# Performance work log

Measured on AMD Instinct MI355X. Metric: run time of the kernel, lower is better.

## Reference

```python
import jax, jax.numpy as jnp
import numpy as np

B, T, C, H = 2, 2048, 768, 12
HD = C // H  # head dim = 64
EPS = 1e-5


def layer_norm(x, g, b):
    mu = jnp.mean(x, axis=-1, keepdims=True)
    var = jnp.var(x, axis=-1, keepdims=True)
    return (x - mu) * jax.lax.rsqrt(var + EPS) * g + b


def setup_inputs() -> dict:
    key = jax.random.key(0)
    ks = jax.random.split(key, 5)
    s = 0.02
    return {
        "x": jax.random.normal(ks[0], (B, T, C), jnp.float32),
        "ln1_g": jnp.ones((C,), jnp.float32),
        "ln1_b": jnp.zeros((C,), jnp.float32),
        "W_qkv": jax.random.normal(ks[1], (C, 3 * C), jnp.float32) * s,
        "W_attn_proj": jax.random.normal(ks[2], (C, C), jnp.float32) * s,
        "ln2_g": jnp.ones((C,), jnp.float32),
        "ln2_b": jnp.zeros((C,), jnp.float32),
        "W_fc": jax.random.normal(ks[3], (C, 4 * C), jnp.float32) * s,
        "W_mlp_proj": jax.random.normal(ks[4], (4 * C, C), jnp.float32) * s,
    }


def attention(x, W_qkv, W_attn_proj):
    b, t, c = x.shape
    qkv = x @ W_qkv  # [B,T,3C]
    q, k, v = jnp.split(qkv, 3, axis=-1)
    # [B,H,T,HD]
    q = q.reshape(b, t, H, HD).transpose(0, 2, 1, 3)
    k = k.reshape(b, t, H, HD).transpose(0, 2, 1, 3)
    v = v.reshape(b, t, H, HD).transpose(0, 2, 1, 3)
    att = jnp.einsum("bhqd,bhkd->bhqk", q, k) * (1.0 / np.sqrt(HD).astype(np.float32))
    causal = jnp.tril(jnp.ones((t, t), jnp.bool_))
    att = jnp.where(causal, att, jnp.finfo(att.dtype).min)
    att = jax.nn.softmax(att, axis=-1)
    y = jnp.einsum("bhqk,bhkd->bhqd", att, v)
    y = y.transpose(0, 2, 1, 3).reshape(b, t, c)
    return y @ W_attn_proj


def mlp(x, W_fc, W_mlp_proj):
    h = jax.nn.gelu(x @ W_fc, approximate=False)
    return h @ W_mlp_proj


def reference(x, ln1_g, ln1_b, W_qkv, W_attn_proj, ln2_g, ln2_b, W_fc, W_mlp_proj):
    x = x + attention(layer_norm(x, ln1_g, ln1_b), W_qkv, W_attn_proj)
    x = x + mlp(layer_norm(x, ln2_g, ln2_b), W_fc, W_mlp_proj)
    return x
```

## Files before the change

kernel.cpp:

```cpp
#include <hip/hip_runtime.h>
#include <cstdint>
#include <cstddef>

typedef unsigned short u16;
typedef __attribute__((ext_vector_type(4))) float f32x4;
typedef __attribute__((ext_vector_type(8))) short bf16x8;

__device__ __forceinline__ u16 f2bf(float f) {
  unsigned int u = __builtin_bit_cast(unsigned int, f);
  u += 0x7fffu + ((u >> 16) & 1u);
  return (u16)(u >> 16);
}

__device__ __forceinline__ void gl_lds16(const u16* g, u16* lds_base) {
  __builtin_amdgcn_global_load_lds(
      (const __attribute__((address_space(1))) unsigned int*)g,
      (__attribute__((address_space(3))) unsigned int*)lds_base, 16, 0, 0);
}

__global__ __launch_bounds__(256) void transpose_all(const float* __restrict__ s0,
                                                     const float* __restrict__ s1,
                                                     const float* __restrict__ s2,
                                                     const float* __restrict__ s3,
                                                     u16* __restrict__ d0,
                                                     u16* __restrict__ d1,
                                                     u16* __restrict__ d2,
                                                     u16* __restrict__ d3) {
  __shared__ float tile[32][33];
  int idx = blockIdx.x;
  const float* src; u16* dst; int K, N, t;
  if (idx < 1728)      { src = s0; dst = d0; K = 768;  N = 2304; t = idx; }
  else if (idx < 2304) { src = s1; dst = d1; K = 768;  N = 768;  t = idx - 1728; }
  else if (idx < 4608) { src = s2; dst = d2; K = 768;  N = 3072; t = idx - 2304; }
  else                 { src = s3; dst = d3; K = 3072; N = 768;  t = idx - 4608; }
  int nt_n = N >> 5;
  int n0 = (t % nt_n) * 32, k0 = (t / nt_n) * 32;
  int tx = threadIdx.x & 31, ty = threadIdx.x >> 5;
#pragma unroll
  for (int i = 0; i < 4; ++i)
    tile[ty + i * 8][tx] = src[(size_t)(k0 + ty + i * 8) * N + n0 + tx];
  __syncthreads();
#pragma unroll
  for (int i = 0; i < 4; ++i)
    dst[(size_t)(n0 + ty + i * 8) * K + k0 + tx] = f2bf(tile[tx][ty + i * 8]);
}

__global__ __launch_bounds__(256) void transpose_v(const u16* __restrict__ qkvb,
                                                   u16* __restrict__ vt,
                                                   unsigned int* __restrict__ ctr) {
  __shared__ u16 tile[64 * 72];
  if (blockIdx.x == 0 && blockIdx.y == 0 && threadIdx.x == 0) *ctr = 0u;
  int t0 = blockIdx.x * 64;
  int bh = blockIdx.y;
  int b = bh / 12, h = bh % 12;
  int tid = threadIdx.x;
  int c8 = tid & 7, r = tid >> 3;
#pragma unroll
  for (int i = 0; i < 2; ++i) {
    int rr = r + i * 32;
    *(uint4*)&tile[rr * 72 + c8 * 8] =
        *(const uint4*)&qkvb[(size_t)(b * 2048 + t0 + rr) * 2304 + 1536 + h * 64 + c8 * 8];
  }
  __syncthreads();
#pragma unroll
  for (int i = 0; i < 2; ++i) {
    int dr = r + i * 32;
    u16 tmp[8];
#pragma unroll
    for (int j = 0; j < 8; ++j) tmp[j] = tile[(c8 * 8 + j) * 72 + dr];
    *(uint4*)&vt[((size_t)bh * 64 + dr) * 2048 + t0 + c8 * 8] = *(uint4*)tmp;
  }
}

__global__ __launch_bounds__(192) void ln_rows(const float* __restrict__ x,
                                               const float* __restrict__ g,
                                               const float* __restrict__ bb,
                                               u16* __restrict__ out) {
  int row = blockIdx.x;
  int t = threadIdx.x;
  float4 v = *(const float4*)(x + (size_t)row * 768 + t * 4);
  float s = v.x + v.y + v.z + v.w;
  float sq = v.x * v.x + v.y * v.y + v.z * v.z + v.w * v.w;
#pragma unroll
  for (int o = 32; o > 0; o >>= 1) {
    s += __shfl_down(s, o);
    sq += __shfl_down(sq, o);
  }
  __shared__ float ss[3], s2[3];
  int w = t >> 6;
  if ((t & 63) == 0) { ss[w] = s; s2[w] = sq; }
  __syncthreads();
  s = ss[0] + ss[1] + ss[2];
  sq = s2[0] + s2[1] + s2[2];
  float mu = s * (1.f / 768.f);
  float var = sq * (1.f / 768.f) - mu * mu;
  float rs = rsqrtf(var + 1e-5f);
  float4 gv = *(const float4*)(g + t * 4);
  float4 bv = *(const float4*)(bb + t * 4);
  u16 o4[4];
  o4[0] = f2bf((v.x - mu) * rs * gv.x + bv.x);
  o4[1] = f2bf((v.y - mu) * rs * gv.y + bv.y);
  o4[2] = f2bf((v.z - mu) * rs * gv.z + bv.z);
  o4[3] = f2bf((v.w - mu) * rs * gv.w + bv.w);
  *(uint2*)(out + (size_t)row * 768 + t * 4) = *(uint2*)o4;
}

template <int EPI, int TM>
__global__ __launch_bounds__(256, 3) void gemm_bt(const u16* __restrict__ A,
                                                  const u16* __restrict__ BT,
                                                  int M, int N, int K,
                                                  float* __restrict__ outF,
                                                  u16* __restrict__ outB,
                                                  const float* __restrict__ res) {
  constexpr int MT = TM / 64;
  __shared__ __align__(16) u16 Al[2][TM * 64];
  __shared__ __align__(16) u16 Bl[2][64 * 64];
  int tid = threadIdx.x;
  int lane = tid & 63, w = tid >> 6;
  int l16 = lane & 15, quad = lane >> 4;
  int swz = l16 & 7;

  int gx = gridDim.x;
  int nwg = gx * gridDim.y;
  int wg = blockIdx.y * gx + blockIdx.x;
  int chunk = nwg >> 3;
  int swg = (wg & 7) * chunk + (wg >> 3);
  int bx = swg % gx, by = swg / gx;

  size_t rowA0 = (size_t)by * TM;
  size_t rowB0 = (size_t)bx * 64;

  auto stage = [&](int buf, int k0) {
#pragma unroll
    for (int i = 0; i < TM / 32; ++i) {
      int cbase = (i * 4 + w) * 64;
      int chunk2 = cbase + lane;
      int r = chunk2 >> 3, c8 = (chunk2 & 7) ^ (r & 7);
      gl_lds16(&A[(rowA0 + r) * (size_t)K + k0 + c8 * 8], &Al[buf][cbase * 8]);
    }
#pragma unroll
    for (int i = 0; i < 2; ++i) {
      int cbase = (i * 4 + w) * 64;
      int chunk2 = cbase + lane;
      int r = chunk2 >> 3, c8 = (chunk2 & 7) ^ (r & 7);
      gl_lds16(&BT[(rowB0 + r) * (size_t)K + k0 + c8 * 8], &Bl[buf][cbase * 8]);
    }
  };

  f32x4 acc[MT][4] = {};
  stage(0, 0);
  int cur = 0;
  for (int k0 = 0; k0 < K; k0 += 64) {
    __syncthreads();
    if (k0 + 64 < K) stage(cur ^ 1, k0 + 64);
#pragma unroll
    for (int ks = 0; ks < 2; ++ks) {
      int c = ks * 4 + quad;
      bf16x8 af[MT], bf[4];
#pragma unroll
      for (int mt = 0; mt < MT; ++mt)
        af[mt] = *(const bf16x8*)&Al[cur][(w * (TM / 4) + mt * 16 + l16) * 64 + (c ^ swz) * 8];
#pragma unroll
      for (int nt = 0; nt < 4; ++nt)
        bf[nt] = *(const bf16x8*)&Bl[cur][(nt * 16 + l16) * 64 + (c ^ swz) * 8];
#pragma unroll
      for (int mt = 0; mt < MT; ++mt)
#pragma unroll
        for (int nt = 0; nt < 4; ++nt)
          acc[mt][nt] = __builtin_amdgcn_mfma_f32_16x16x32_bf16(af[mt], bf[nt], acc[mt][nt], 0, 0, 0);
    }
    cur ^= 1;
  }

#pragma unroll
  for (int mt = 0; mt < MT; ++mt) {
#pragma unroll
    for (int i = 0; i < 4; ++i) {
      size_t row = rowA0 + w * (TM / 4) + mt * 16 + quad * 4 + i;
#pragma unroll
      for (int nt = 0; nt < 4; ++nt) {
        size_t col = rowB0 + nt * 16 + l16;
        float v = acc[mt][nt][i];
        if (EPI == 0) {
          outB[row * N + col] = f2bf(v);
        } else if (EPI == 1) {
          outF[row * N + col] = res[row * N + col] + v;
        } else {
          float ge = 0.5f * v * (1.f + erff(v * 0.70710678118654752f));
          outB[row * N + col] = f2bf(ge);
        }
      }
    }
  }
}

__global__ __launch_bounds__(256, 3) void flash_attn(const u16* __restrict__ qkv,
                                                     const u16* __restrict__ vt,
                                                     u16* __restrict__ y,
                                                     float* __restrict__ OP,
                                                     float* __restrict__ LP,
                                                     unsigned int* __restrict__ ctr) {
  __shared__ __align__(16) u16 Kl[128 * 64];
  __shared__ __align__(16) u16 Vl[64 * 128];
  __shared__ __align__(16) u16 Pl[4][16 * 136];
  __shared__ unsigned int s_unit;

  int tid = threadIdx.x;
  int lane = tid & 63, w = tid >> 6;
  int l16 = lane & 15, quad = lane >> 4;
  int swz = l16 & 7;
  u16* Pw = &Pl[w][0];

  for (;;) {
    __syncthreads();
    if (tid == 0) s_unit = atomicAdd(ctr, 1u);
    __syncthreads();
    unsigned int u = s_unit;
    if (u >= 1152u) return;

    int qt, bh, kb0, kb1, part;
    bool heavy;
    if (u < 384u) {
      int t = (int)u;
      qt = 31 - t / 24; bh = t % 24;
      part = 0; kb0 = 0; kb1 = 8; heavy = true;
    } else if (u < 768u) {
      int t = (int)u - 384;
      qt = 31 - t / 24; bh = t % 24;
      part = 1; kb0 = 8; kb1 = qt / 2 + 1; heavy = true;
    } else {
      int t = (int)u - 768;
      qt = 15 - t / 24; bh = t % 24;
      part = 0; kb0 = 0; kb1 = qt / 2 + 1; heavy = false;
    }
    int b = bh / 12, h = bh % 12;
    int qw = qt * 64 + w * 16;
    int kdiag = qt / 2;

    const u16* base = qkv + (size_t)b * 2048 * 2304;
    const u16* vbase = vt + (size_t)bh * 64 * 2048;

    bf16x8 qf0, qf1;
    {
      const u16* qp = base + (size_t)(qw + l16) * 2304 + h * 64 + quad * 8;
      qf0 = *(const bf16x8*)qp;
      qf1 = *(const bf16x8*)(qp + 32);
    }

    f32x4 O[4] = {};
    float l_i[4] = {0.f, 0.f, 0.f, 0.f};

    const float sc = 0.125f * 1.44269504088896340736f;

    auto stageK = [&](int kt0) {
#pragma unroll
      for (int i = 0; i < 4; ++i) {
        int cbase = (i * 4 + w) * 64;
        int chunk = cbase + lane;
        int r = chunk >> 3, c8 = (chunk & 7) ^ (r & 7);
        gl_lds16(base + (size_t)(kt0 + r) * 2304 + 768 + h * 64 + c8 * 8, &Kl[cbase * 8]);
      }
    };
    auto stageV = [&](int kt0) {
#pragma unroll
      for (int i = 0; i < 4; ++i) {
        int cbase = (i * 4 + w) * 64;
        int chunk = cbase + lane;
        int r = chunk >> 4, c16 = (chunk & 15) ^ (r & 7);
        gl_lds16(vbase + (size_t)r * 2048 + kt0 + c16 * 8, &Vl[cbase * 8]);
      }
    };

    stageK(kb0 << 7);
    for (int kb = kb0; kb < kb1; ++kb) {
      int kt0 = kb << 7;
      __syncthreads();
      stageV(kt0);

      f32x4 S[8];
#pragma unroll
      for (int nt = 0; nt < 8; ++nt) {
        bf16x8 k0 = *(const bf16x8*)&Kl[(nt * 16 + l16) * 64 + (quad ^ swz) * 8];
        bf16x8 k1 = *(const bf16x8*)&Kl[(nt * 16 + l16) * 64 + ((4 + quad) ^ swz) * 8];
        f32x4 z = {};
        z = __builtin_amdgcn_mfma_f32_16x16x32_bf16(qf0, k0, z, 0, 0, 0);
        S[nt] = __builtin_amdgcn_mfma_f32_16x16x32_bf16(qf1, k1, z, 0, 0, 0);
      }

      bool diag = (kb == kdiag);
#pragma unroll
      for (int nt = 0; nt < 8; ++nt) {
        int tk = kt0 + nt * 16 + l16;
#pragma unroll
        for (int i = 0; i < 4; ++i) {
          float p = exp2f(S[nt][i] * sc);
          if (diag && tk > qw + quad * 4 + i) p = 0.f;
          l_i[i] += p;
          Pw[(quad * 4 + i) * 136 + nt * 16 + l16] =
              (u16)(__builtin_bit_cast(unsigned int, p) >> 16);
        }
      }

      __syncthreads();
      if (kb + 1 < kb1) stageK((kb + 1) << 7);

#pragma unroll
      for (int c = 0; c < 4; ++c) {
        bf16x8 pf = *(const bf16x8*)&Pw[l16 * 136 + c * 32 + quad * 8];
#pragma unroll
        for (int dt = 0; dt < 4; ++dt) {
          bf16x8 vf = *(const bf16x8*)&Vl[(dt * 16 + l16) * 128 + ((c * 4 + quad) ^ swz) * 8];
          O[dt] = __builtin_amdgcn_mfma_f32_16x16x32_bf16(pf, vf, O[dt], 0, 0, 0);
        }
      }
    }

#pragma unroll
    for (int i = 0; i < 4; ++i) {
#pragma unroll
      for (int o = 1; o < 16; o <<= 1) l_i[i] += __shfl_xor(l_i[i], o);
    }

    if (heavy) {
      size_t tno = (size_t)(bh * 16 + (qt - 16)) * 2 + part;
      float* op = OP + tno * 4096;
      float* lp = LP + tno * 64;
#pragma unroll
      for (int dt = 0; dt < 4; ++dt) {
#pragma unroll
        for (int i = 0; i < 4; ++i)
          op[(w * 16 + quad * 4 + i) * 64 + dt * 16 + l16] = O[dt][i];
      }
      if (l16 == 0) {
#pragma unroll
        for (int i = 0; i < 4; ++i) lp[w * 16 + quad * 4 + i] = l_i[i];
      }
    } else {
#pragma unroll
      for (int dt = 0; dt < 4; ++dt) {
#pragma unroll
        for (int i = 0; i < 4; ++i) {
          int tq = qw + quad * 4 + i;
          float ov = O[dt][i] / l_i[i];
          y[(size_t)(b * 2048 + tq) * 768 + h * 64 + dt * 16 + l16] = f2bf(ov);
        }
      }
    }
  }
}

__global__ __launch_bounds__(256) void attn_combine(const float* __restrict__ OP,
                                                    const float* __restrict__ LP,
                                                    u16* __restrict__ y) {
  int t = blockIdx.x;
  int bh = t >> 4, qth = t & 15;
  int b = bh / 12, h = bh % 12;
  int tid = threadIdx.x;
  int r = tid >> 2;
  int c0 = (tid & 3) << 4;
  const float* a = OP + (size_t)t * 2 * 4096 + r * 64 + c0;
  const float* bp = a + 4096;
  float inv = 1.f / (LP[(size_t)t * 128 + r] + LP[(size_t)t * 128 + 64 + r]);
  u16 ob[16];
#pragma unroll
  for (int j = 0; j < 16; ++j) ob[j] = f2bf((a[j] + bp[j]) * inv);
  size_t row = (size_t)b * 2048 + (size_t)(16 + qth) * 64 + r;
  u16* yp = y + row * 768 + h * 64 + c0;
  *(uint4*)yp = *(uint4*)&ob[0];
  *(uint4*)(yp + 8) = *(uint4*)&ob[8];
}

extern "C" void kernel_launch(void* const* d_in, const int* in_sizes, int n_in,
                              void* d_out, int out_size, void* d_ws, size_t ws_size,
                              hipStream_t stream) {
  const float* x      = (const float*)d_in[0];
  const float* ln1_g  = (const float*)d_in[1];
  const float* ln1_b  = (const float*)d_in[2];
  const float* W_qkv  = (const float*)d_in[3];
  const float* W_attn = (const float*)d_in[4];
  const float* ln2_g  = (const float*)d_in[5];
  const float* ln2_b  = (const float*)d_in[6];
  const float* W_fc   = (const float*)d_in[7];
  const float* W_mlp  = (const float*)d_in[8];
  float* out = (float*)d_out;

  const int M = 4096;
  char* p = (char*)d_ws;
  auto alloc = [&](size_t bytes) {
    char* r = p;
    p += (bytes + 255) & ~(size_t)255;
    return r;
  };
  u16* wt_qkv  = (u16*)alloc((size_t)2304 * 768 * 2);
  u16* wt_attn = (u16*)alloc((size_t)768 * 768 * 2);
  u16* wt_fc   = (u16*)alloc((size_t)3072 * 768 * 2);
  u16* wt_mlp  = (u16*)alloc((size_t)768 * 3072 * 2);
  u16* xn1     = (u16*)alloc((size_t)M * 768 * 2);
  u16* qkvb    = (u16*)alloc((size_t)M * 2304 * 2);
  u16* yb      = (u16*)alloc((size_t)M * 768 * 2);
  float* x1    = (float*)alloc((size_t)M * 768 * 4);
  u16* xn2     = (u16*)alloc((size_t)M * 768 * 2);
  u16* hb      = (u16*)alloc((size_t)M * 3072 * 2);
  u16* vt      = (u16*)alloc((size_t)24 * 64 * 2048 * 2);
  unsigned int* ctr = (unsigned int*)alloc(256);

  float* OPb = (float*)hb;
  float* LPb = OPb + (size_t)24 * 16 * 2 * 4096;

  transpose_all<<<6912, 256, 0, stream>>>(W_qkv, W_attn, W_fc, W_mlp,
                                          wt_qkv, wt_attn, wt_fc, wt_mlp);

  ln_rows<<<M, 192, 0, stream>>>(x, ln1_g, ln1_b, xn1);
  gemm_bt<0, 128><<<dim3(2304 / 64, M / 128), 256, 0, stream>>>(xn1, wt_qkv, M, 2304, 768,
                                                                nullptr, qkvb, nullptr);
  transpose_v<<<dim3(32, 24), 256, 0, stream>>>(qkvb, vt, ctr);
  flash_attn<<<768, 256, 0, stream>>>(qkvb, vt, yb, OPb, LPb, ctr);
  attn_combine<<<384, 256, 0, stream>>>(OPb, LPb, yb);
  gemm_bt<1, 64><<<dim3(768 / 64, M / 64), 256, 0, stream>>>(yb, wt_attn, M, 768, 768,
                                                             x1, nullptr, x);
  ln_rows<<<M, 192, 0, stream>>>(x1, ln2_g, ln2_b, xn2);
  gemm_bt<2, 128><<<dim3(3072 / 64, M / 128), 256, 0, stream>>>(xn2, wt_fc, M, 3072, 768,
                                                                nullptr, hb, nullptr);
  gemm_bt<1, 64><<<dim3(768 / 64, M / 64), 256, 0, stream>>>(hb, wt_mlp, M, 768, 3072,
                                                             out, nullptr, x1);
}
```

Baseline: 267.6 us.

## Add 128x128 tiled GEMM with XCD-aware block swizzle for QKV and FC projections

Introduces a new gemm_sq kernel that uses 128x128 output tiles with a 2x2 wave layout, so each wave computes a 64x64 sub-tile. It also remaps workgroup IDs into eight chunks so neighbouring tiles land on the same XCD, which should improve L2 reuse. The QKV and FC projections switch to this kernel, halving the grid size and increasing data reuse per loaded tile. The trade-off is more accumulator registers per thread and fewer workgroups, which may reduce occupancy and tail balance on 256 CUs.

```diff
diff --git a/kernel.cpp b/kernel.cpp
--- a/kernel.cpp
+++ b/kernel.cpp
@@ -185,6 +185,91 @@
           outB[row * N + col] = f2bf(v);
         } else if (EPI == 1) {
           outF[row * N + col] = res[row * N + col] + v;
+        } else {
+          float ge = 0.5f * v * (1.f + erff(v * 0.70710678118654752f));
+          outB[row * N + col] = f2bf(ge);
+        }
+      }
+    }
+  }
+}
+
+template <int EPI>
+__global__ __launch_bounds__(256, 2) void gemm_sq(const u16* __restrict__ A,
+                                                  const u16* __restrict__ BT,
+                                                  int M, int N, int K,
+                                                  u16* __restrict__ outB) {
+  __shared__ __align__(16) u16 Al[2][128 * 64];
+  __shared__ __align__(16) u16 Bl[2][128 * 64];
+  int tid = threadIdx.x;
+  int lane = tid & 63, w = tid >> 6;
+  int l16 = lane & 15, quad = lane >> 4;
+  int swz = l16 & 7;
+  int wr = w >> 1, wc = w & 1;
+
+  int gx = gridDim.x;
+  int nwg = gx * gridDim.y;
+  int wg = blockIdx.y * gx + blockIdx.x;
+  int chunk = nwg >> 3;
+  int swg = (wg & 7) * chunk + (wg >> 3);
+  int bx = swg % gx, by = swg / gx;
+
+  size_t rowA0 = (size_t)by * 128;
+  size_t rowB0 = (size_t)bx * 128;
+
+  auto stage = [&](int buf, int k0) {
+#pragma unroll
+    for (int i = 0; i < 4; ++i) {
+      int cbase = (i * 4 + w) * 64;
+      int chunk2 = cbase + lane;
+      int r = chunk2 >> 3, c8 = (chunk2 & 7) ^ (r & 7);
+      gl_lds16(&A[(rowA0 + r) * (size_t)K + k0 + c8 * 8], &Al[buf][cbase * 8]);
+    }
+#pragma unroll
+    for (int i = 0; i < 4; ++i) {
+      int cbase = (i * 4 + w) * 64;
+      int chunk2 = cbase + lane;
+      int r = chunk2 >> 3, c8 = (chunk2 & 7) ^ (r & 7);
+      gl_lds16(&BT[(rowB0 + r) * (size_t)K + k0 + c8 * 8], &Bl[buf][cbase * 8]);
+    }
+  };
+
+  f32x4 acc[4][4] = {};
+  stage(0, 0);
+  int cur = 0;
+  for (int k0 = 0; k0 < K; k0 += 64) {
+    __syncthreads();
+    if (k0 + 64 < K) stage(cur ^ 1, k0 + 64);
+#pragma unroll
+    for (int ks = 0; ks < 2; ++ks) {
+      int c = ks * 4 + quad;
+      bf16x8 af[4], bf[4];
+#pragma unroll
+      for (int mt = 0; mt < 4; ++mt)
+        af[mt] = *(const bf16x8*)&Al[cur][(wr * 64 + mt * 16 + l16) * 64 + (c ^ swz) * 8];
+#pragma unroll
+      for (int nt = 0; nt < 4; ++nt)
+        bf[nt] = *(const bf16x8*)&Bl[cur][(wc * 64 + nt * 16 + l16) * 64 + (c ^ swz) * 8];
+#pragma unroll
+      for (int mt = 0; mt < 4; ++mt)
+#pragma unroll
+        for (int nt = 0; nt < 4; ++nt)
+          acc[mt][nt] = __builtin_amdgcn_mfma_f32_16x16x32_bf16(af[mt], bf[nt], acc[mt][nt], 0, 0, 0);
+    }
+    cur ^= 1;
+  }
+
+#pragma unroll
+  for (int mt = 0; mt < 4; ++mt) {
+#pragma unroll
+    for (int i = 0; i < 4; ++i) {
+      size_t row = rowA0 + wr * 64 + mt * 16 + quad * 4 + i;
+#pragma unroll
+      for (int nt = 0; nt < 4; ++nt) {
+        size_t col = rowB0 + wc * 64 + nt * 16 + l16;
+        float v = acc[mt][nt][i];
+        if (EPI == 0) {
+          outB[row * N + col] = f2bf(v);
         } else {
           float ge = 0.5f * v * (1.f + erff(v * 0.70710678118654752f));
           outB[row * N + col] = f2bf(ge);
@@ -411,16 +496,16 @@
                                           wt_qkv, wt_attn, wt_fc, wt_mlp);
 
   ln_rows<<<M, 192, 0, stream>>>(x, ln1_g, ln1_b, xn1);
-  gemm_bt<0, 128><<<dim3(2304 / 64, M / 128), 256, 0, stream>>>(xn1, wt_qkv, M, 2304, 768,
-                                                                nullptr, qkvb, nullptr);
+  gemm_sq<0><<<dim3(2304 / 128, M / 128), 256, 0, stream>>>(xn1, wt_qkv, M, 2304, 768,
+                                                            qkvb);
   transpose_v<<<dim3(32, 24), 256, 0, stream>>>(qkvb, vt, ctr);
   flash_attn<<<768, 256, 0, stream>>>(qkvb, vt, yb, OPb, LPb, ctr);
   attn_combine<<<384, 256, 0, stream>>>(OPb, LPb, yb);
   gemm_bt<1, 64><<<dim3(768 / 64, M / 64), 256, 0, stream>>>(yb, wt_attn, M, 768, 768,
                                                              x1, nullptr, x);
   ln_rows<<<M, 192, 0, stream>>>(x1, ln2_g, ln2_b, xn2);
-  gemm_bt<2, 128><<<dim3(3072 / 64, M / 128), 256, 0, stream>>>(xn2, wt_fc, M, 3072, 768,
-                                                                nullptr, hb, nullptr);
+  gemm_sq<2><<<dim3(3072 / 128, M / 128), 256, 0, stream>>>(xn2, wt_fc, M, 3072, 768,
+                                                            hb);
   gemm_bt<1, 64><<<dim3(768 / 64, M / 64), 256, 0, stream>>>(hb, wt_mlp, M, 768, 3072,
                                                              out, nullptr, x1);
 }
```

New measurement: 276.3 us. 1.03x slower.

## Shrink flash-attention key tiles to 64 and split-K into 512-key chunks

Applied to the files above, without the earlier changes.

Flash attention now processes 64-key blocks instead of 128, so causal diagonal work is masked at a finer grain and less of it is wasted. Long query tiles (qt≥8) are split into up to four 512-key partial units, with a new schedule ordering work units and a combine kernel that sums up to four partials. The smaller LDS footprint allows raising the occupancy hint from 3 to 6 blocks, and the grid is doubled. In exchange there are more partial writes and reads of fp32 outputs, more scheduling atomics, and more loop iterations with per-iteration barriers. The partial buffer is moved to span the x1/xn2/hb workspace.

```diff
diff --git a/kernel.cpp b/kernel.cpp
--- a/kernel.cpp
+++ b/kernel.cpp
@@ -194,15 +194,15 @@
   }
 }
 
-__global__ __launch_bounds__(256, 3) void flash_attn(const u16* __restrict__ qkv,
+__global__ __launch_bounds__(256, 6) void flash_attn(const u16* __restrict__ qkv,
                                                      const u16* __restrict__ vt,
                                                      u16* __restrict__ y,
                                                      float* __restrict__ OP,
                                                      float* __restrict__ LP,
                                                      unsigned int* __restrict__ ctr) {
-  __shared__ __align__(16) u16 Kl[128 * 64];
-  __shared__ __align__(16) u16 Vl[64 * 128];
-  __shared__ __align__(16) u16 Pl[4][16 * 136];
+  __shared__ __align__(16) u16 Kl[64 * 64];
+  __shared__ __align__(16) u16 Vl[64 * 64];
+  __shared__ __align__(16) u16 Pl[4][16 * 72];
   __shared__ unsigned int s_unit;
 
   int tid = threadIdx.x;
@@ -216,26 +216,27 @@
     if (tid == 0) s_unit = atomicAdd(ctr, 1u);
     __syncthreads();
     unsigned int u = s_unit;
-    if (u >= 1152u) return;
-
-    int qt, bh, kb0, kb1, part;
-    bool heavy;
-    if (u < 384u) {
-      int t = (int)u;
-      qt = 31 - t / 24; bh = t % 24;
-      part = 0; kb0 = 0; kb1 = 8; heavy = true;
-    } else if (u < 768u) {
-      int t = (int)u - 384;
-      qt = 31 - t / 24; bh = t % 24;
-      part = 1; kb0 = 8; kb1 = qt / 2 + 1; heavy = true;
+    if (u >= 1920u) return;
+
+    int qt, bh, kb0, kb1, j;
+    if (u < 1248u) {
+      bh = (int)(u % 24u);
+      int fi = (int)(u / 24u);
+      qt = 31;
+      for (;;) { int nf = (qt + 1) >> 3; if (fi < nf) break; fi -= nf; --qt; }
+      j = fi; kb0 = j * 8; kb1 = kb0 + 8;
     } else {
-      int t = (int)u - 768;
-      qt = 15 - t / 24; bh = t % 24;
-      part = 0; kb0 = 0; kb1 = qt / 2 + 1; heavy = false;
-    }
+      int ti = (int)u - 1248;
+      bh = ti % 24;
+      int k = ti / 24;
+      int s = 7 - (k >> 2);
+      qt = 8 * (3 - (k & 3)) + s - 1;
+      j = (qt + 1) >> 3;
+      kb0 = j * 8; kb1 = qt + 1;
+    }
+    bool multi = (qt >= 8);
     int b = bh / 12, h = bh % 12;
     int qw = qt * 64 + w * 16;
-    int kdiag = qt / 2;
 
     const u16* base = qkv + (size_t)b * 2048 * 2304;
     const u16* vbase = vt + (size_t)bh * 64 * 2048;
@@ -249,12 +250,11 @@
 
     f32x4 O[4] = {};
     float l_i[4] = {0.f, 0.f, 0.f, 0.f};
-
     const float sc = 0.125f * 1.44269504088896340736f;
 
     auto stageK = [&](int kt0) {
 #pragma unroll
-      for (int i = 0; i < 4; ++i) {
+      for (int i = 0; i < 2; ++i) {
         int cbase = (i * 4 + w) * 64;
         int chunk = cbase + lane;
         int r = chunk >> 3, c8 = (chunk & 7) ^ (r & 7);
@@ -263,23 +263,23 @@
     };
     auto stageV = [&](int kt0) {
 #pragma unroll
-      for (int i = 0; i < 4; ++i) {
+      for (int i = 0; i < 2; ++i) {
         int cbase = (i * 4 + w) * 64;
         int chunk = cbase + lane;
-        int r = chunk >> 4, c16 = (chunk & 15) ^ (r & 7);
-        gl_lds16(vbase + (size_t)r * 2048 + kt0 + c16 * 8, &Vl[cbase * 8]);
+        int r = chunk >> 3, c8 = (chunk & 7) ^ (r & 7);
+        gl_lds16(vbase + (size_t)r * 2048 + kt0 + c8 * 8, &Vl[cbase * 8]);
       }
     };
 
-    stageK(kb0 << 7);
+    stageK(kb0 << 6);
     for (int kb = kb0; kb < kb1; ++kb) {
-      int kt0 = kb << 7;
+      int kt0 = kb << 6;
       __syncthreads();
       stageV(kt0);
 
-      f32x4 S[8];
-#pragma unroll
-      for (int nt = 0; nt < 8; ++nt) {
+      f32x4 S[4];
+#pragma unroll
+      for (int nt = 0; nt < 4; ++nt) {
         bf16x8 k0 = *(const bf16x8*)&Kl[(nt * 16 + l16) * 64 + (quad ^ swz) * 8];
         bf16x8 k1 = *(const bf16x8*)&Kl[(nt * 16 + l16) * 64 + ((4 + quad) ^ swz) * 8];
         f32x4 z = {};
@@ -287,29 +287,29 @@
         S[nt] = __builtin_amdgcn_mfma_f32_16x16x32_bf16(qf1, k1, z, 0, 0, 0);
       }
 
-      bool diag = (kb == kdiag);
-#pragma unroll
-      for (int nt = 0; nt < 8; ++nt) {
+      bool diag = (kb == qt);
+#pragma unroll
+      for (int nt = 0; nt < 4; ++nt) {
         int tk = kt0 + nt * 16 + l16;
 #pragma unroll
         for (int i = 0; i < 4; ++i) {
           float p = exp2f(S[nt][i] * sc);
           if (diag && tk > qw + quad * 4 + i) p = 0.f;
           l_i[i] += p;
-          Pw[(quad * 4 + i) * 136 + nt * 16 + l16] =
+          Pw[(quad * 4 + i) * 72 + nt * 16 + l16] =
               (u16)(__builtin_bit_cast(unsigned int, p) >> 16);
         }
       }
 
       __syncthreads();
-      if (kb + 1 < kb1) stageK((kb + 1) << 7);
-
-#pragma unroll
-      for (int c = 0; c < 4; ++c) {
-        bf16x8 pf = *(const bf16x8*)&Pw[l16 * 136 + c * 32 + quad * 8];
+      if (kb + 1 < kb1) stageK((kb + 1) << 6);
+
+#pragma unroll
+      for (int c = 0; c < 2; ++c) {
+        bf16x8 pf = *(const bf16x8*)&Pw[l16 * 72 + c * 32 + quad * 8];
 #pragma unroll
         for (int dt = 0; dt < 4; ++dt) {
-          bf16x8 vf = *(const bf16x8*)&Vl[(dt * 16 + l16) * 128 + ((c * 4 + quad) ^ swz) * 8];
+          bf16x8 vf = *(const bf16x8*)&Vl[(dt * 16 + l16) * 64 + ((c * 4 + quad) ^ swz) * 8];
           O[dt] = __builtin_amdgcn_mfma_f32_16x16x32_bf16(pf, vf, O[dt], 0, 0, 0);
         }
       }
@@ -321,10 +321,10 @@
       for (int o = 1; o < 16; o <<= 1) l_i[i] += __shfl_xor(l_i[i], o);
     }
 
-    if (heavy) {
-      size_t tno = (size_t)(bh * 16 + (qt - 16)) * 2 + part;
-      float* op = OP + tno * 4096;
-      float* lp = LP + tno * 64;
+    if (multi) {
+      size_t slot = ((size_t)bh * 24 + (qt - 8)) * 4 + j;
+      float* op = OP + slot * 4096;
+      float* lp = LP + slot * 64;
 #pragma unroll
       for (int dt = 0; dt < 4; ++dt) {
 #pragma unroll
@@ -353,18 +353,29 @@
                                                     const float* __restrict__ LP,
                                                     u16* __restrict__ y) {
   int t = blockIdx.x;
-  int bh = t >> 4, qth = t & 15;
+  int bh = t / 24, qtm = t % 24;
+  int qt = qtm + 8;
   int b = bh / 12, h = bh % 12;
+  int np = (qt + 8) >> 3;
   int tid = threadIdx.x;
   int r = tid >> 2;
   int c0 = (tid & 3) << 4;
-  const float* a = OP + (size_t)t * 2 * 4096 + r * 64 + c0;
-  const float* bp = a + 4096;
-  float inv = 1.f / (LP[(size_t)t * 128 + r] + LP[(size_t)t * 128 + 64 + r]);
+  const float* basep = OP + (size_t)t * 4 * 4096 + r * 64 + c0;
+  float acc[16];
+#pragma unroll
+  for (int jj = 0; jj < 16; ++jj) acc[jj] = 0.f;
+  float lsum = 0.f;
+  for (int pp = 0; pp < np; ++pp) {
+    const float* a = basep + pp * 4096;
+    lsum += LP[((size_t)t * 4 + pp) * 64 + r];
+#pragma unroll
+    for (int jj = 0; jj < 16; ++jj) acc[jj] += a[jj];
+  }
+  float inv = 1.f / lsum;
   u16 ob[16];
 #pragma unroll
-  for (int j = 0; j < 16; ++j) ob[j] = f2bf((a[j] + bp[j]) * inv);
-  size_t row = (size_t)b * 2048 + (size_t)(16 + qth) * 64 + r;
+  for (int jj = 0; jj < 16; ++jj) ob[jj] = f2bf(acc[jj] * inv);
+  size_t row = (size_t)b * 2048 + (size_t)qt * 64 + r;
   u16* yp = y + row * 768 + h * 64 + c0;
   *(uint4*)yp = *(uint4*)&ob[0];
   *(uint4*)(yp + 8) = *(uint4*)&ob[8];
@@ -404,8 +415,8 @@
   u16* vt      = (u16*)alloc((size_t)24 * 64 * 2048 * 2);
   unsigned int* ctr = (unsigned int*)alloc(256);
 
-  float* OPb = (float*)hb;
-  float* LPb = OPb + (size_t)24 * 16 * 2 * 4096;
+  float* OPb = x1;
+  float* LPb = OPb + (size_t)2304 * 4096;
 
   transpose_all<<<6912, 256, 0, stream>>>(W_qkv, W_attn, W_fc, W_mlp,
                                           wt_qkv, wt_attn, wt_fc, wt_mlp);
@@ -414,8 +425,8 @@
   gemm_bt<0, 128><<<dim3(2304 / 64, M / 128), 256, 0, stream>>>(xn1, wt_qkv, M, 2304, 768,
                                                                 nullptr, qkvb, nullptr);
   transpose_v<<<dim3(32, 24), 256, 0, stream>>>(qkvb, vt, ctr);
-  flash_attn<<<768, 256, 0, stream>>>(qkvb, vt, yb, OPb, LPb, ctr);
-  attn_combine<<<384, 256, 0, stream>>>(OPb, LPb, yb);
+  flash_attn<<<1536, 256, 0, stream>>>(qkvb, vt, yb, OPb, LPb, ctr);
+  attn_combine<<<576, 256, 0, stream>>>(OPb, LPb, yb);
   gemm_bt<1, 64><<<dim3(768 / 64, M / 64), 256, 0, stream>>>(yb, wt_attn, M, 768, 768,
                                                              x1, nullptr, x);
   ln_rows<<<M, 192, 0, stream>>>(x1, ln2_g, ln2_b, xn2);
```

Measured after the change: 283.6 us. +6.0%, slower.

## Keep attention probabilities in registers via transposed MFMA and lane shuffles

Applied to the files above, without the earlier changes.

Swaps the MFMA operand order so S and O are computed transposed, which puts each query row along lanes. The P tile is then packed to bf16 in registers and redistributed with shuffles instead of a per-wave LDS round trip. This removes the Pl shared buffer, which allows raising launch bounds to 4 blocks per CU and the persistent grid to 1024. The row-sum reduction and output stores become simpler and vectorized, at the cost of many shuffles per chunk and possible register pressure under the tighter occupancy bound.

```diff
diff --git a/kernel.cpp b/kernel.cpp
--- a/kernel.cpp
+++ b/kernel.cpp
@@ -5,6 +5,7 @@
 typedef unsigned short u16;
 typedef __attribute__((ext_vector_type(4))) float f32x4;
 typedef __attribute__((ext_vector_type(8))) short bf16x8;
+typedef __attribute__((ext_vector_type(4))) unsigned int u32x4;
 
 __device__ __forceinline__ u16 f2bf(float f) {
   unsigned int u = __builtin_bit_cast(unsigned int, f);
@@ -194,7 +195,7 @@
   }
 }
 
-__global__ __launch_bounds__(256, 3) void flash_attn(const u16* __restrict__ qkv,
+__global__ __launch_bounds__(256, 4) void flash_attn(const u16* __restrict__ qkv,
                                                      const u16* __restrict__ vt,
                                                      u16* __restrict__ y,
                                                      float* __restrict__ OP,
@@ -202,14 +203,12 @@
                                                      unsigned int* __restrict__ ctr) {
   __shared__ __align__(16) u16 Kl[128 * 64];
   __shared__ __align__(16) u16 Vl[64 * 128];
-  __shared__ __align__(16) u16 Pl[4][16 * 136];
   __shared__ unsigned int s_unit;
 
   int tid = threadIdx.x;
   int lane = tid & 63, w = tid >> 6;
   int l16 = lane & 15, quad = lane >> 4;
   int swz = l16 & 7;
-  u16* Pw = &Pl[w][0];
 
   for (;;) {
     __syncthreads();
@@ -236,6 +235,7 @@
     int b = bh / 12, h = bh % 12;
     int qw = qt * 64 + w * 16;
     int kdiag = qt / 2;
+    int qg = qw + l16;
 
     const u16* base = qkv + (size_t)b * 2048 * 2304;
     const u16* vbase = vt + (size_t)bh * 64 * 2048;
@@ -248,8 +248,7 @@
     }
 
     f32x4 O[4] = {};
-    float l_i[4] = {0.f, 0.f, 0.f, 0.f};
-
+    float lsum = 0.f;
     const float sc = 0.125f * 1.44269504088896340736f;
 
     auto stageK = [&](int kt0) {
@@ -271,6 +270,10 @@
       }
     };
 
+    int sA = ((quad & 1) << 5) + l16;
+    int sB = sA + 16;
+    bool hiq = quad >= 2;
+
     stageK(kb0 << 7);
     for (int kb = kb0; kb < kb1; ++kb) {
       int kt0 = kb << 7;
@@ -283,22 +286,25 @@
         bf16x8 k0 = *(const bf16x8*)&Kl[(nt * 16 + l16) * 64 + (quad ^ swz) * 8];
         bf16x8 k1 = *(const bf16x8*)&Kl[(nt * 16 + l16) * 64 + ((4 + quad) ^ swz) * 8];
         f32x4 z = {};
-        z = __builtin_amdgcn_mfma_f32_16x16x32_bf16(qf0, k0, z, 0, 0, 0);
-        S[nt] = __builtin_amdgcn_mfma_f32_16x16x32_bf16(qf1, k1, z, 0, 0, 0);
+        z = __builtin_amdgcn_mfma_f32_16x16x32_bf16(k0, qf0, z, 0, 0, 0);
+        S[nt] = __builtin_amdgcn_mfma_f32_16x16x32_bf16(k1, qf1, z, 0, 0, 0);
       }
 
       bool diag = (kb == kdiag);
+      unsigned int pw0[8], pw1[8];
 #pragma unroll
       for (int nt = 0; nt < 8; ++nt) {
-        int tk = kt0 + nt * 16 + l16;
+        float pp[4];
 #pragma unroll
         for (int i = 0; i < 4; ++i) {
           float p = exp2f(S[nt][i] * sc);
-          if (diag && tk > qw + quad * 4 + i) p = 0.f;
-          l_i[i] += p;
-          Pw[(quad * 4 + i) * 136 + nt * 16 + l16] =
-              (u16)(__builtin_bit_cast(unsigned int, p) >> 16);
+          int tok = kt0 + nt * 16 + quad * 4 + i;
+          if (diag && tok > qg) p = 0.f;
+          lsum += p;
+          pp[i] = p;
         }
+        pw0[nt] = (unsigned int)f2bf(pp[0]) | ((unsigned int)f2bf(pp[1]) << 16);
+        pw1[nt] = (unsigned int)f2bf(pp[2]) | ((unsigned int)f2bf(pp[3]) << 16);
       }
 
       __syncthreads();
@@ -306,44 +312,48 @@
 
 #pragma unroll
       for (int c = 0; c < 4; ++c) {
-        bf16x8 pf = *(const bf16x8*)&Pw[l16 * 136 + c * 32 + quad * 8];
+        int a0 = __shfl((int)pw0[2 * c], sA);
+        int a1 = __shfl((int)pw1[2 * c], sA);
+        int a2 = __shfl((int)pw0[2 * c], sB);
+        int a3 = __shfl((int)pw1[2 * c], sB);
+        int b0 = __shfl((int)pw0[2 * c + 1], sA);
+        int b1 = __shfl((int)pw1[2 * c + 1], sA);
+        int b2 = __shfl((int)pw0[2 * c + 1], sB);
+        int b3 = __shfl((int)pw1[2 * c + 1], sB);
+        u32x4 bw;
+        bw.x = hiq ? (unsigned int)b0 : (unsigned int)a0;
+        bw.y = hiq ? (unsigned int)b1 : (unsigned int)a1;
+        bw.z = hiq ? (unsigned int)b2 : (unsigned int)a2;
+        bw.w = hiq ? (unsigned int)b3 : (unsigned int)a3;
+        bf16x8 pB = __builtin_bit_cast(bf16x8, bw);
 #pragma unroll
         for (int dt = 0; dt < 4; ++dt) {
           bf16x8 vf = *(const bf16x8*)&Vl[(dt * 16 + l16) * 128 + ((c * 4 + quad) ^ swz) * 8];
-          O[dt] = __builtin_amdgcn_mfma_f32_16x16x32_bf16(pf, vf, O[dt], 0, 0, 0);
+          O[dt] = __builtin_amdgcn_mfma_f32_16x16x32_bf16(vf, pB, O[dt], 0, 0, 0);
         }
       }
     }
 
-#pragma unroll
-    for (int i = 0; i < 4; ++i) {
-#pragma unroll
-      for (int o = 1; o < 16; o <<= 1) l_i[i] += __shfl_xor(l_i[i], o);
-    }
+    lsum += __shfl_xor(lsum, 16);
+    lsum += __shfl_xor(lsum, 32);
 
     if (heavy) {
       size_t tno = (size_t)(bh * 16 + (qt - 16)) * 2 + part;
       float* op = OP + tno * 4096;
       float* lp = LP + tno * 64;
 #pragma unroll
+      for (int dt = 0; dt < 4; ++dt)
+        *(f32x4*)&op[(w * 16 + l16) * 64 + dt * 16 + quad * 4] = O[dt];
+      if (quad == 0) lp[w * 16 + l16] = lsum;
+    } else {
+      float inv = 1.f / lsum;
+#pragma unroll
       for (int dt = 0; dt < 4; ++dt) {
-#pragma unroll
-        for (int i = 0; i < 4; ++i)
-          op[(w * 16 + quad * 4 + i) * 64 + dt * 16 + l16] = O[dt][i];
-      }
-      if (l16 == 0) {
-#pragma unroll
-        for (int i = 0; i < 4; ++i) lp[w * 16 + quad * 4 + i] = l_i[i];
-      }
-    } else {
-#pragma unroll
-      for (int dt = 0; dt < 4; ++dt) {
-#pragma unroll
-        for (int i = 0; i < 4; ++i) {
-          int tq = qw + quad * 4 + i;
-          float ov = O[dt][i] / l_i[i];
-          y[(size_t)(b * 2048 + tq) * 768 + h * 64 + dt * 16 + l16] = f2bf(ov);
-        }
+        u16 ob[4];
+#pragma unroll
+        for (int i = 0; i < 4; ++i) ob[i] = f2bf(O[dt][i] * inv);
+        *(uint2*)&y[(size_t)(b * 2048 + qg) * 768 + h * 64 + dt * 16 + quad * 4] =
+            *(uint2*)ob;
       }
     }
   }
@@ -414,7 +424,7 @@
   gemm_bt<0, 128><<<dim3(2304 / 64, M / 128), 256, 0, stream>>>(xn1, wt_qkv, M, 2304, 768,
                                                                 nullptr, qkvb, nullptr);
   transpose_v<<<dim3(32, 24), 256, 0, stream>>>(qkvb, vt, ctr);
-  flash_attn<<<768, 256, 0, stream>>>(qkvb, vt, yb, OPb, LPb, ctr);
+  flash_attn<<<1024, 256, 0, stream>>>(qkvb, vt, yb, OPb, LPb, ctr);
   attn_combine<<<384, 256, 0, stream>>>(OPb, LPb, yb);
   gemm_bt<1, 64><<<dim3(768 / 64, M / 64), 256, 0, stream>>>(yb, wt_attn, M, 768, 768,
                                                              x1, nullptr, x);
```

After: 283.2 us. +5.8%, slower.
